# Performance work log

Measured on AMD Instinct MI355X. Metric: run time of the kernel, lower is better.

The kernel has to match this reference:

```python
import jax, jax.numpy as jnp
import numpy as np
import math

# dims: batch, tgt_len, img_feat, wordvec, heads, vocab, layers, ffn
N, T, D, W, H, V, L, FF = 8, 512, 1024, 512, 4, 32000, 2, 2048
NULL = 0  # padding_idx -> zero embedding row


def _pos_encoding(max_len, dim):
    pos = jnp.arange(max_len, dtype=jnp.float32)[:, None]
    j = jnp.arange(dim)[None, :]
    je = (j - (j % 2)).astype(jnp.float32)
    ang = pos * jnp.power(10000.0, -je / dim)
    return jnp.where(j % 2 == 0, jnp.sin(ang), jnp.cos(ang))  # (max_len, dim)


def setup_inputs() -> dict:
    key = jax.random.key(0)
    ks = iter(jax.random.split(key, 80))

    def nrm(shape):
        return jax.random.normal(next(ks), shape, jnp.float32) * 0.02

    inp = {}
    inp["features"] = jax.random.normal(next(ks), (N, D), jnp.float32)
    inp["captions"] = jax.random.randint(next(ks), (N, T), 0, V)
    emb = nrm((V, W)).at[NULL].set(0.0)  # padding_idx row zeroed
    inp["emb"] = emb
    inp["pe"] = _pos_encoding(T, W)
    inp["vis_w"] = nrm((D, W)); inp["vis_b"] = jnp.zeros((W,), jnp.float32)
    for p in ["sa", "ca"]:
        for q in ["q", "k", "v", "o"]:
            inp[f"{p}_w{q}"] = nrm((L, W, W))
            inp[f"{p}_b{q}"] = jnp.zeros((L, W), jnp.float32)
    inp["ff1_w"] = nrm((L, W, FF)); inp["ff1_b"] = jnp.zeros((L, FF), jnp.float32)
    inp["ff2_w"] = nrm((L, FF, W)); inp["ff2_b"] = jnp.zeros((L, W), jnp.float32)
    for i in (1, 2, 3):
        inp[f"ln{i}_w"] = jnp.ones((L, W), jnp.float32)
        inp[f"ln{i}_b"] = jnp.zeros((L, W), jnp.float32)
    inp["out_w"] = nrm((W, V)); inp["out_b"] = jnp.zeros((V,), jnp.float32)
    return inp


def _layer_norm(x, w, b):
    m = x.mean(-1, keepdims=True)
    v = ((x - m) ** 2).mean(-1, keepdims=True)
    return (x - m) / jnp.sqrt(v + 1e-5) * w + b


def _mha(qx, kx, vx, wq, bq, wk, bk, wv, bv, wo, bo, mask):
    n, s, e = qx.shape
    t = kx.shape[1]
    d = e // H
    q = (qx @ wq + bq).reshape(n, s, H, d)
    k = (kx @ wk + bk).reshape(n, t, H, d)
    v = (vx @ wv + bv).reshape(n, t, H, d)
    a = jnp.einsum("nshd,nthd->nhst", q, k) / math.sqrt(d)  # (N,H,S,T)
    if mask is not None:
        a = jnp.where(mask, a, -jnp.inf)
    e_ = jax.nn.softmax(a, axis=-1)
    y = jnp.einsum("nhst,nthd->nshd", e_, v).reshape(n, s, e)
    return y @ wo + bo


def reference(features, captions, emb, pe, vis_w, vis_b,
              sa_wq, sa_bq, sa_wk, sa_bk, sa_wv, sa_bv, sa_wo, sa_bo,
              ca_wq, ca_bq, ca_wk, ca_bk, ca_wv, ca_bv, ca_wo, ca_bo,
              ff1_w, ff1_b, ff2_w, ff2_b,
              ln1_w, ln1_b, ln2_w, ln2_b, ln3_w, ln3_b, out_w, out_b):
    memory = (features @ vis_w + vis_b)[:, None, :]  # (N,1,W)
    t_len = captions.shape[1]
    x = emb[captions] + pe[None, :t_len, :]  # (N,T,W)
    mask = jnp.tril(jnp.ones((t_len, t_len), bool))  # causal tgt_mask
    for l in range(L):
        t2 = _mha(x, x, x, sa_wq[l], sa_bq[l], sa_wk[l], sa_bk[l],
                  sa_wv[l], sa_bv[l], sa_wo[l], sa_bo[l], mask)
        x = _layer_norm(x + t2, ln1_w[l], ln1_b[l])
        t2 = _mha(x, memory, memory, ca_wq[l], ca_bq[l], ca_wk[l], ca_bk[l],
                  ca_wv[l], ca_bv[l], ca_wo[l], ca_bo[l], None)
        x = _layer_norm(x + t2, ln2_w[l], ln2_b[l])
        t2 = jax.nn.relu(x @ ff1_w[l] + ff1_b[l]) @ ff2_w[l] + ff2_b[l]
        x = _layer_norm(x + t2, ln3_w[l], ln3_b[l])
    return x @ out_w + out_b  # (N,T,V)
```

## Files before the change

### kernel.cpp

```cpp
#include <hip/hip_runtime.h>
#include <math.h>

#define WDIM   512
#define TLEN   512
#define NBATCH 8
#define NHEADS 4
#define DHEAD  128
#define VOCAB  32000
#define NLAY   2
#define FFDIM  2048
#define DFEAT  1024
#define NT     (NBATCH * TLEN)
#define QKVW   (3 * WDIM)

typedef unsigned short u16;
typedef __attribute__((ext_vector_type(8))) short bf16x8;
typedef __attribute__((ext_vector_type(4))) float f32x4;

__device__ inline u16 f2bf(float f) {
    union { float f; unsigned u; } v; v.f = f;
    unsigned r = v.u + 0x7fffu + ((v.u >> 16) & 1u);
    return (u16)(r >> 16);
}
__device__ inline u16 to_bf(float f) { return f2bf(f); }
__device__ inline u16 to_bf(u16 v)  { return v; }

__global__ __launch_bounds__(256)
void cvt_kernel(const float* __restrict__ s, u16* __restrict__ d, int n)
{
    int i = blockIdx.x * 256 + threadIdx.x;
    if (i < n) d[i] = f2bf(s[i]);
}

__global__ __launch_bounds__(256)
void concat_bias_kernel(const float* __restrict__ bq, const float* __restrict__ bk,
                        const float* __restrict__ bv, float* __restrict__ dst)
{
    int i = blockIdx.x * 256 + threadIdx.x;
    if (i >= NLAY * QKVW) return;
    int l = i / QKVW, j = i - l * QKVW;
    float v = (j < WDIM) ? bq[l * WDIM + j]
            : (j < 2 * WDIM) ? bk[l * WDIM + j - WDIM]
            : bv[l * WDIM + j - 2 * WDIM];
    dst[i] = v;
}

template<typename T>
__global__ __launch_bounds__(256)
void transpose_cvt_kernel(const T* __restrict__ src, int lds_, long ssn, long ssh,
                          u16* __restrict__ dst, int ldd, long dsn, long dsh,
                          int HH)
{
    int z = blockIdx.z;
    int zn = z / HH, zh = z - zn * HH;
    src += (long)zn * ssn + (long)zh * ssh;
    dst += (long)zn * dsn + (long)zh * dsh;
    __shared__ T tile[32][33];
    int n0 = blockIdx.x * 32, k0 = blockIdx.y * 32;
    int tx = threadIdx.x & 31, ty = threadIdx.x >> 5;
    #pragma unroll
    for (int i = 0; i < 32; i += 8)
        tile[ty + i][tx] = src[(long)(k0 + ty + i) * lds_ + n0 + tx];
    __syncthreads();
    #pragma unroll
    for (int i = 0; i < 32; i += 8)
        dst[(long)(n0 + ty + i) * ldd + k0 + tx] = to_bf(tile[tx][ty + i]);
}

__global__ __launch_bounds__(128)
void embed_kernel(const int* __restrict__ captions, const float* __restrict__ emb,
                  const float* __restrict__ pe, float* __restrict__ x, u16* __restrict__ xb)
{
    int r = blockIdx.x;
    int t = r % TLEN;
    int cap = captions[r];
    const float4* e4 = (const float4*)(emb + (long)cap * WDIM);
    const float4* p4 = (const float4*)(pe + (long)t * WDIM);
    float4 a = e4[threadIdx.x], b = p4[threadIdx.x];
    float4 o = make_float4(a.x + b.x, a.y + b.y, a.z + b.z, a.w + b.w);
    ((float4*)(x + (long)r * WDIM))[threadIdx.x] = o;
    ushort4 ob = make_ushort4(f2bf(o.x), f2bf(o.y), f2bf(o.z), f2bf(o.w));
    ((ushort4*)(xb + (long)r * WDIM))[threadIdx.x] = ob;
}

#define GBM 128
#define GBN 128
#define GBK 32

template<int RELU, int NTST, int CAUSAL>
__global__ __launch_bounds__(256)
void mfma_gemm_kernel(const u16* __restrict__ A, int lda, long sAn, long sAh,
                      const u16* __restrict__ B, int ldb, long sBn, long sBh,
                      float* __restrict__ C, u16* __restrict__ Cb, int ldc, long sCn, long sCh,
                      const float* __restrict__ bias, long sbias,
                      int M, int N, int K, int HH, float alpha)
{
    int z = blockIdx.z;
    int zn = z / HH, zh = z - zn * HH;
    A += (long)zn * sAn + (long)zh * sAh;
    B += (long)zn * sBn + (long)zh * sBh;
    long coff = (long)zn * sCn + (long)zh * sCh;
    if (bias) bias += (long)zn * sbias;

    int nwg  = gridDim.x * gridDim.y;
    int orig = blockIdx.y * gridDim.x + blockIdx.x;
    int q = nwg >> 3, r = nwg & 7, xcd = orig & 7, rest = orig >> 3;
    int nw = (xcd < r ? xcd * (q + 1) : r * (q + 1) + (xcd - r) * q) + rest;
    int bx = nw / gridDim.y, by = nw - bx * gridDim.y;
    int bm = by * GBM, bn = bx * GBN;

    if (CAUSAL && bn >= bm + GBM) return;

    __shared__ u16 As[2][GBM * GBK];
    __shared__ u16 Bs[2][GBN * GBK];

    int tid = threadIdx.x;
    int w = tid >> 6, lane = tid & 63;
    int wr = w >> 1, wc = w & 1;
    int lrow = lane & 15, kgrp = lane >> 4;

    int c0row = tid >> 2, c0ko = (tid & 3) << 3;
    long ldsOff = (size_t)(w * 64) * 8;

    auto STAGE = [&](int buf, int ks) {
        int k0 = ks * GBK;
        #pragma unroll
        for (int i = 0; i < 2; i++) {
            int row = c0row + i * 64;
            int gr = bm + row; if (gr >= M) gr = M - 1;
            const u16* srcA = A + (long)gr * lda + k0 + c0ko;
            u16* dstA = &As[buf][ldsOff + (size_t)i * 256 * 8];
            __builtin_amdgcn_global_load_lds((const __attribute__((address_space(1))) void*)srcA,
                                             (__attribute__((address_space(3))) void*)dstA, 16, 0, 0);
            const u16* srcB = B + (long)(bn + row) * ldb + k0 + c0ko;
            u16* dstB = &Bs[buf][ldsOff + (size_t)i * 256 * 8];
            __builtin_amdgcn_global_load_lds((const __attribute__((address_space(1))) void*)srcB,
                                             (__attribute__((address_space(3))) void*)dstB, 16, 0, 0);
        }
    };

    f32x4 acc[4][4] = {};
    int nsteps = K / GBK;

    STAGE(0, 0);

    for (int ks = 0; ks < nsteps; ks++) {
        int cur = ks & 1;
        if (ks + 1 < nsteps) {
            STAGE(cur ^ 1, ks + 1);
            asm volatile("s_waitcnt vmcnt(4)" ::: "memory");
        } else {
            asm volatile("s_waitcnt vmcnt(0)" ::: "memory");
        }
        __builtin_amdgcn_sched_barrier(0);
        __builtin_amdgcn_s_barrier();
        __builtin_amdgcn_sched_barrier(0);
        bf16x8 av[4], bv[4];
        #pragma unroll
        for (int m = 0; m < 4; m++)
            av[m] = *(const bf16x8*)&As[cur][(wr * 64 + m * 16 + lrow) * GBK + kgrp * 8];
        #pragma unroll
        for (int n = 0; n < 4; n++)
            bv[n] = *(const bf16x8*)&Bs[cur][(wc * 64 + n * 16 + lrow) * GBK + kgrp * 8];
        #pragma unroll
        for (int m = 0; m < 4; m++)
            #pragma unroll
            for (int n = 0; n < 4; n++)
                acc[m][n] = __builtin_amdgcn_mfma_f32_16x16x32_bf16(av[m], bv[n], acc[m][n], 0, 0, 0);
        __builtin_amdgcn_sched_barrier(0);
        __builtin_amdgcn_s_barrier();
        __builtin_amdgcn_sched_barrier(0);
    }

    if (NTST) {
        __syncthreads();
        float* ls = (float*)&As[0][0];
        C += coff;
        #pragma unroll
        for (int pass = 0; pass < 4; pass++) {
            if (wr == (pass >> 1)) {
                #pragma unroll
                for (int m2 = 0; m2 < 2; m2++) {
                    int m = (pass & 1) * 2 + m2;
                    #pragma unroll
                    for (int n = 0; n < 4; n++) {
                        int gc = wc * 64 + n * 16 + lrow;
                        float bvv = bias ? bias[bn + gc] : 0.f;
                        #pragma unroll
                        for (int r2 = 0; r2 < 4; r2++) {
                            float v2 = acc[m][n][r2] * alpha + bvv;
                            if (RELU) v2 = fmaxf(v2, 0.f);
                            ls[(m2 * 16 + kgrp * 4 + r2) * 128 + gc] = v2;
                        }
                    }
                }
            }
            __syncthreads();
            #pragma unroll
            for (int i = 0; i < 4; i++) {
                int j = tid + i * 256;
                int row = j >> 5, cg = j & 31;
                int gr = bm + pass * 32 + row;
                if (gr < M) {
                    f32x4 v4 = *(const f32x4*)&ls[row * 128 + cg * 4];
                    __builtin_nontemporal_store(v4, (f32x4*)&C[(long)gr * ldc + bn + cg * 4]);
                }
            }
            __syncthreads();
        }
        return;
    }

    if (C)  C  += coff;
    if (Cb) Cb += coff;
    #pragma unroll
    for (int m = 0; m < 4; m++) {
        int rb = bm + wr * 64 + m * 16 + kgrp * 4;
        #pragma unroll
        for (int n = 0; n < 4; n++) {
            int gc = bn + wc * 64 + n * 16 + lrow;
            float bvv = bias ? bias[gc] : 0.f;
            #pragma unroll
            for (int r2 = 0; r2 < 4; r2++) {
                int gr = rb + r2;
                if (gr < M) {
                    float v2 = acc[m][n][r2] * alpha + bvv;
                    if (RELU) v2 = fmaxf(v2, 0.f);
                    if (C)  C[(long)gr * ldc + gc]  = v2;
                    if (Cb) Cb[(long)gr * ldc + gc] = f2bf(v2);
                }
            }
        }
    }
}

__global__ __launch_bounds__(128)
void mfma_gemm_half_kernel(const u16* __restrict__ A, int lda, long sAn, long sAh,
                           const u16* __restrict__ B, int ldb, long sBn, long sBh,
                           float* __restrict__ C, u16* __restrict__ Cb, int ldc, long sCn, long sCh,
                           const float* __restrict__ bias,
                           int M, int N, int K, int HH, float alpha)
{
    int z = blockIdx.z;
    int zn = z / HH, zh = z - zn * HH;
    A += (long)zn * sAn + (long)zh * sAh;
    B += (long)zn * sBn + (long)zh * sBh;
    long coff = (long)zn * sCn + (long)zh * sCh;

    int nwg  = gridDim.x * gridDim.y;
    int orig = blockIdx.y * gridDim.x + blockIdx.x;
    int q = nwg >> 3, r = nwg & 7, xcd = orig & 7, rest = orig >> 3;
    int nw = (xcd < r ? xcd * (q + 1) : r * (q + 1) + (xcd - r) * q) + rest;
    int bx = nw / gridDim.y, by = nw - bx * gridDim.y;
    int bm = by * 128, bn = bx * 64;

    __shared__ u16 As[2][128 * GBK];
    __shared__ u16 Bs[2][64 * GBK];

    int tid = threadIdx.x;
    int w = tid >> 6, lane = tid & 63;
    int lrow = lane & 15, kgrp = lane >> 4;

    auto STAGE = [&](int buf, int ks) {
        int k0 = ks * GBK;
        #pragma unroll
        for (int i = 0; i < 4; i++) {
            int c = tid + i * 128;
            int row = c >> 2, ko2 = (c & 3) << 3;
            int gr = bm + row; if (gr >= M) gr = M - 1;
            const u16* srcA = A + (long)gr * lda + k0 + ko2;
            u16* dstA = &As[buf][(size_t)(i * 128 + w * 64) * 8];
            __builtin_amdgcn_global_load_lds((const __attribute__((address_space(1))) void*)srcA,
                                             (__attribute__((address_space(3))) void*)dstA, 16, 0, 0);
        }
        #pragma unroll
        for (int i = 0; i < 2; i++) {
            int c = tid + i * 128;
            int row = c >> 2, ko2 = (c & 3) << 3;
            const u16* srcB = B + (long)(bn + row) * ldb + k0 + ko2;
            u16* dstB = &Bs[buf][(size_t)(i * 128 + w * 64) * 8];
            __builtin_amdgcn_global_load_lds((const __attribute__((address_space(1))) void*)srcB,
                                             (__attribute__((address_space(3))) void*)dstB, 16, 0, 0);
        }
    };

    f32x4 acc[4][4] = {};
    int nsteps = K / GBK;

    STAGE(0, 0);

    for (int ks = 0; ks < nsteps; ks++) {
        int cur = ks & 1;
        if (ks + 1 < nsteps) {
            STAGE(cur ^ 1, ks + 1);
            asm volatile("s_waitcnt vmcnt(6)" ::: "memory");
        } else {
            asm volatile("s_waitcnt vmcnt(0)" ::: "memory");
        }
        __builtin_amdgcn_sched_barrier(0);
        __builtin_amdgcn_s_barrier();
        __builtin_amdgcn_sched_barrier(0);
        bf16x8 av[4], bv[4];
        #pragma unroll
        for (int m = 0; m < 4; m++)
            av[m] = *(const bf16x8*)&As[cur][(w * 64 + m * 16 + lrow) * GBK + kgrp * 8];
        #pragma unroll
        for (int n = 0; n < 4; n++)
            bv[n] = *(const bf16x8*)&Bs[cur][(n * 16 + lrow) * GBK + kgrp * 8];
        #pragma unroll
        for (int m = 0; m < 4; m++)
            #pragma unroll
            for (int n = 0; n < 4; n++)
                acc[m][n] = __builtin_amdgcn_mfma_f32_16x16x32_bf16(av[m], bv[n], acc[m][n], 0, 0, 0);
        __builtin_amdgcn_sched_barrier(0);
        __builtin_amdgcn_s_barrier();
        __builtin_amdgcn_sched_barrier(0);
    }

    if (C)  C  += coff;
    if (Cb) Cb += coff;
    #pragma unroll
    for (int m = 0; m < 4; m++) {
        int rb = bm + w * 64 + m * 16 + kgrp * 4;
        #pragma unroll
        for (int n = 0; n < 4; n++) {
            int gc = bn + n * 16 + lrow;
            float bvv = bias ? bias[gc] : 0.f;
            #pragma unroll
            for (int r2 = 0; r2 < 4; r2++) {
                int gr = rb + r2;
                if (gr < M) {
                    float v2 = acc[m][n][r2] * alpha + bvv;
                    if (C)  C[(long)gr * ldc + gc]  = v2;
                    if (Cb) Cb[(long)gr * ldc + gc] = f2bf(v2);
                }
            }
        }
    }
}

__global__ __launch_bounds__(256)
void softmax_causal_kernel(const float* __restrict__ scores, u16* __restrict__ pb)
{
    long row = blockIdx.x;
    int s = (int)(row % TLEN);
    const float* p = scores + row * TLEN;
    u16* o = pb + row * TLEN;
    int tid = threadIdx.x;
    float v0 = p[tid], v1 = p[tid + 256];
    bool m0 = (tid <= s), m1 = (tid + 256 <= s);
    __shared__ float red[256];
    float mx = fmaxf(m0 ? v0 : -INFINITY, m1 ? v1 : -INFINITY);
    red[tid] = mx; __syncthreads();
    for (int off = 128; off > 0; off >>= 1) {
        if (tid < off) red[tid] = fmaxf(red[tid], red[tid + off]);
        __syncthreads();
    }
    mx = red[0]; __syncthreads();
    float e0 = m0 ? expf(v0 - mx) : 0.f;
    float e1 = m1 ? expf(v1 - mx) : 0.f;
    red[tid] = e0 + e1; __syncthreads();
    for (int off = 128; off > 0; off >>= 1) {
        if (tid < off) red[tid] += red[tid + off];
        __syncthreads();
    }
    float inv = 1.f / red[0];
    o[tid]       = f2bf(e0 * inv);
    o[tid + 256] = f2bf(e1 * inv);
}

__device__ inline void ln_pass(float& v0, float& v1, const float* __restrict__ w,
                               const float* __restrict__ b, float* red, int tid)
{
    red[tid] = v0 + v1; __syncthreads();
    for (int off = 128; off > 0; off >>= 1) {
        if (tid < off) red[tid] += red[tid + off];
        __syncthreads();
    }
    float mean = red[0] * (1.f / WDIM); __syncthreads();
    float d0 = v0 - mean, d1 = v1 - mean;
    red[tid] = d0 * d0 + d1 * d1; __syncthreads();
    for (int off = 128; off > 0; off >>= 1) {
        if (tid < off) red[tid] += red[tid + off];
        __syncthreads();
    }
    float rstd = 1.f / sqrtf(red[0] * (1.f / WDIM) + 1e-5f);
    __syncthreads();
    v0 = d0 * rstd * w[tid] + b[tid];
    v1 = d1 * rstd * w[tid + 256] + b[tid + 256];
}

__global__ __launch_bounds__(256)
void add_ln_kernel(float* __restrict__ x, u16* __restrict__ xb,
                   const float* __restrict__ t2,
                   const float* __restrict__ w, const float* __restrict__ b)
{
    long r = blockIdx.x;
    float* xr = x + r * WDIM;
    u16* xbr = xb + r * WDIM;
    const float* tr = t2 + r * WDIM;
    int tid = threadIdx.x;
    float v0 = xr[tid] + tr[tid];
    float v1 = xr[tid + 256] + tr[tid + 256];
    __shared__ float red[256];
    ln_pass(v0, v1, w, b, red, tid);
    xr[tid] = v0;        xr[tid + 256] = v1;
    xbr[tid] = f2bf(v0); xbr[tid + 256] = f2bf(v1);
}

__global__ __launch_bounds__(256)
void add_ln2_kernel(float* __restrict__ x, u16* __restrict__ xb,
                    const float* __restrict__ t2, const float* __restrict__ cav,
                    const float* __restrict__ w1, const float* __restrict__ b1,
                    const float* __restrict__ w2, const float* __restrict__ b2)
{
    long r = blockIdx.x;
    float* xr = x + r * WDIM;
    u16* xbr = xb + r * WDIM;
    const float* tr = t2 + r * WDIM;
    const float* cr = cav + (r / TLEN) * WDIM;
    int tid = threadIdx.x;
    float v0 = xr[tid] + tr[tid];
    float v1 = xr[tid + 256] + tr[tid + 256];
    __shared__ float red[256];
    ln_pass(v0, v1, w1, b1, red, tid);
    __syncthreads();
    v0 += cr[tid]; v1 += cr[tid + 256];
    ln_pass(v0, v1, w2, b2, red, tid);
    xr[tid] = v0;        xr[tid + 256] = v1;
    xbr[tid] = f2bf(v0); xbr[tid + 256] = f2bf(v1);
}

extern "C" void kernel_launch(void* const* d_in, const int* in_sizes, int n_in,
                              void* d_out, int out_size, void* d_ws, size_t ws_size,
                              hipStream_t stream)
{
    const float* features = (const float*)d_in[0];
    const int*   captions = (const int*)  d_in[1];
    const float* emb      = (const float*)d_in[2];
    const float* pe       = (const float*)d_in[3];
    const float* vis_w    = (const float*)d_in[4];
    const float* vis_b    = (const float*)d_in[5];
    const float* sa_wq    = (const float*)d_in[6];
    const float* sa_bq    = (const float*)d_in[7];
    const float* sa_wk    = (const float*)d_in[8];
    const float* sa_bk    = (const float*)d_in[9];
    const float* sa_wv    = (const float*)d_in[10];
    const float* sa_bv    = (const float*)d_in[11];
    const float* sa_wo    = (const float*)d_in[12];
    const float* sa_bo    = (const float*)d_in[13];
    const float* ca_wv    = (const float*)d_in[18];
    const float* ca_bv    = (const float*)d_in[19];
    const float* ca_wo    = (const float*)d_in[20];
    const float* ca_bo    = (const float*)d_in[21];
    const float* ff1_w    = (const float*)d_in[22];
    const float* ff1_b    = (const float*)d_in[23];
    const float* ff2_w    = (const float*)d_in[24];
    const float* ff2_b    = (const float*)d_in[25];
    const float* ln1_w    = (const float*)d_in[26];
    const float* ln1_b    = (const float*)d_in[27];
    const float* ln2_w    = (const float*)d_in[28];
    const float* ln2_b    = (const float*)d_in[29];
    const float* ln3_w    = (const float*)d_in[30];
    const float* ln3_b    = (const float*)d_in[31];
    const float* out_w    = (const float*)d_in[32];
    const float* out_b    = (const float*)d_in[33];

    char* p = (char*)d_ws;
    auto alloc = [&](size_t bytes) { char* r = p; p += (bytes + 255) & ~(size_t)255; return r; };
    float* x    = (float*)alloc((size_t)NT * WDIM * 4);
    float* t2   = (float*)alloc((size_t)NT * WDIM * 4);
    float* memb = (float*)alloc((size_t)NBATCH * WDIM * 4);
    float* cav  = (float*)alloc((size_t)NLAY * NBATCH * WDIM * 4);
    char*  reg1 = alloc((size_t)NBATCH * NHEADS * TLEN * TLEN * 4);
    float* scores = (float*)reg1;
    u16*   yb     = (u16*)reg1;
    u16*   hb     = (u16*)reg1;
    u16* xb    = (u16*)alloc((size_t)NT * WDIM * 2);
    u16* qkvb  = (u16*)alloc((size_t)NT * QKVW * 2);
    u16* vtb   = (u16*)alloc((size_t)NT * WDIM * 2);
    u16* pb    = (u16*)alloc((size_t)NBATCH * NHEADS * TLEN * TLEN * 2);
    u16* featb = (u16*)alloc((size_t)NBATCH * DFEAT * 2);
    u16* membf = (u16*)alloc((size_t)NBATCH * WDIM * 2);
    u16* cvb   = (u16*)alloc((size_t)NLAY * NBATCH * WDIM * 2);
    float* qkv_bias = (float*)alloc((size_t)NLAY * QKVW * 4);
    u16* vis_wT = (u16*)alloc((size_t)WDIM * DFEAT * 2);
    u16* qkvT   = (u16*)alloc((size_t)NLAY * QKVW * WDIM * 2);
    u16* sa_woT = (u16*)alloc((size_t)NLAY * WDIM * WDIM * 2);
    u16* ca_wvT = (u16*)alloc((size_t)NLAY * WDIM * WDIM * 2);
    u16* ca_woT = (u16*)alloc((size_t)NLAY * WDIM * WDIM * 2);
    u16* ff1T   = (u16*)alloc((size_t)NLAY * WDIM * FFDIM * 2);
    u16* ff2T   = (u16*)alloc((size_t)NLAY * FFDIM * WDIM * 2);
    u16* out_wT = (u16*)alloc((size_t)WDIM * VOCAB * 2);

    auto gemm = [&](const u16* A, int lda, long sAn, long sAh,
                    const u16* B, int ldb, long sBn, long sBh,
                    float* C, u16* Cb, int ldc, long sCn, long sCh,
                    const float* bias, long sbias, int M, int N, int K, int HH, int batch,
                    float alpha, int mode)
    {
        dim3 g(N / GBN, (M + GBM - 1) / GBM, batch), blk(256);
        if (mode == 2)
            mfma_gemm_kernel<0, 1, 0><<<g, blk, 0, stream>>>(A, lda, sAn, sAh, B, ldb, sBn, sBh,
                                                             C, Cb, ldc, sCn, sCh, bias, sbias, M, N, K, HH, alpha);
        else if (mode == 1)
            mfma_gemm_kernel<1, 0, 0><<<g, blk, 0, stream>>>(A, lda, sAn, sAh, B, ldb, sBn, sBh,
                                                             C, Cb, ldc, sCn, sCh, bias, sbias, M, N, K, HH, alpha);
        else if (mode == 3)
            mfma_gemm_kernel<0, 0, 1><<<g, blk, 0, stream>>>(A, lda, sAn, sAh, B, ldb, sBn, sBh,
                                                             C, Cb, ldc, sCn, sCh, bias, sbias, M, N, K, HH, alpha);
        else
            mfma_gemm_kernel<0, 0, 0><<<g, blk, 0, stream>>>(A, lda, sAn, sAh, B, ldb, sBn, sBh,
                                                             C, Cb, ldc, sCn, sCh, bias, sbias, M, N, K, HH, alpha);
    };
    auto gemmh = [&](const u16* A, int lda, long sAn, long sAh,
                     const u16* B, int ldb, long sBn, long sBh,
                     float* C, u16* Cb, int ldc, long sCn, long sCh,
                     const float* bias, int M, int N, int K, int HH, int batch,
                     float alpha)
    {
        dim3 g(N / 64, (M + 127) / 128, batch), blk(128);
        mfma_gemm_half_kernel<<<g, blk, 0, stream>>>(A, lda, sAn, sAh, B, ldb, sBn, sBh,
                                                     C, Cb, ldc, sCn, sCh, bias, M, N, K, HH, alpha);
    };
    auto transposeF = [&](const float* src, int lds_, long ssn, long ssh,
                          u16* dst, int ldd, long dsn, long dsh,
                          int K, int N, int batch, int HH)
    {
        dim3 g(N / 32, K / 32, batch), blk(256);
        transpose_cvt_kernel<float><<<g, blk, 0, stream>>>(src, lds_, ssn, ssh, dst, ldd, dsn, dsh, HH);
    };
    auto transposeB = [&](const u16* src, int lds_, long ssn, long ssh,
                          u16* dst, int ldd, long dsn, long dsh,
                          int K, int N, int batch, int HH)
    {
        dim3 g(N / 32, K / 32, batch), blk(256);
        transpose_cvt_kernel<u16><<<g, blk, 0, stream>>>(src, lds_, ssn, ssh, dst, ldd, dsn, dsh, HH);
    };

    cvt_kernel<<<(NBATCH * DFEAT + 255) / 256, 256, 0, stream>>>(features, featb, NBATCH * DFEAT);
    concat_bias_kernel<<<(NLAY * QKVW + 255) / 256, 256, 0, stream>>>(sa_bq, sa_bk, sa_bv, qkv_bias);
    transposeF(vis_w, WDIM, 0, 0, vis_wT, DFEAT, 0, 0, DFEAT, WDIM, 1, 1);
    transposeF(sa_wq, WDIM, (long)WDIM * WDIM, 0, qkvT,                WDIM, (long)QKVW * WDIM, 0, WDIM, WDIM, NLAY, 1);
    transposeF(sa_wk, WDIM, (long)WDIM * WDIM, 0, qkvT + (long)WDIM * WDIM,     WDIM, (long)QKVW * WDIM, 0, WDIM, WDIM, NLAY, 1);
    transposeF(sa_wv, WDIM, (long)WDIM * WDIM, 0, qkvT + (long)2 * WDIM * WDIM, WDIM, (long)QKVW * WDIM, 0, WDIM, WDIM, NLAY, 1);
    transposeF(sa_wo, WDIM, (long)WDIM * WDIM, 0, sa_woT, WDIM, (long)WDIM * WDIM, 0, WDIM, WDIM, NLAY, 1);
    transposeF(ca_wv, WDIM, (long)WDIM * WDIM, 0, ca_wvT, WDIM, (long)WDIM * WDIM, 0, WDIM, WDIM, NLAY, 1);
    transposeF(ca_wo, WDIM, (long)WDIM * WDIM, 0, ca_woT, WDIM, (long)WDIM * WDIM, 0, WDIM, WDIM, NLAY, 1);
    transposeF(ff1_w, FFDIM, (long)WDIM * FFDIM, 0, ff1T, WDIM, (long)FFDIM * WDIM, 0, WDIM, FFDIM, NLAY, 1);
    transposeF(ff2_w, WDIM, (long)FFDIM * WDIM, 0, ff2T, FFDIM, (long)WDIM * FFDIM, 0, FFDIM, WDIM, NLAY, 1);
    transposeF(out_w, VOCAB, 0, 0, out_wT, WDIM, 0, 0, WDIM, VOCAB, 1, 1);

    gemm(featb, DFEAT, 0, 0, vis_wT, DFEAT, 0, 0, memb, membf, WDIM, 0, 0,
         vis_b, 0, NBATCH, WDIM, DFEAT, 1, 1, 1.f, 0);
    embed_kernel<<<NT, 128, 0, stream>>>(captions, emb, pe, x, xb);

    gemm(membf, WDIM, 0, 0, ca_wvT, WDIM, (long)WDIM * WDIM, 0,
         nullptr, cvb, WDIM, (long)NBATCH * WDIM, 0,
         ca_bv, WDIM, NBATCH, WDIM, WDIM, 1, NLAY, 1.f, 0);
    gemm(cvb, WDIM, (long)NBATCH * WDIM, 0, ca_woT, WDIM, (long)WDIM * WDIM, 0,
         cav, nullptr, WDIM, (long)NBATCH * WDIM, 0,
         ca_bo, WDIM, NBATCH, WDIM, WDIM, 1, NLAY, 1.f, 0);

    const float iscale = 1.f / sqrtf((float)DHEAD);
    const long TQ = (long)TLEN * QKVW;
    const long TW = (long)TLEN * WDIM;
    const long TT = (long)TLEN * TLEN;
    for (int l = 0; l < NLAY; l++) {
        long wo  = (long)l * WDIM * WDIM;
        long bo_ = (long)l * WDIM;
        gemm(xb, WDIM, 0, 0, qkvT + (long)l * QKVW * WDIM, WDIM, 0, 0,
             nullptr, qkvb, QKVW, 0, 0, qkv_bias + (long)l * QKVW, 0,
             NT, QKVW, WDIM, 1, 1, 1.f, 0);
        transposeB(qkvb + 2 * WDIM, QKVW, TQ, DHEAD,
                   vtb, TLEN, (long)NHEADS * DHEAD * TLEN, (long)DHEAD * TLEN,
                   TLEN, DHEAD, NBATCH * NHEADS, NHEADS);
        gemm(qkvb, QKVW, TQ, DHEAD, qkvb + WDIM, QKVW, TQ, DHEAD,
             scores, nullptr, TLEN, (long)NHEADS * TT, TT,
             nullptr, 0, TLEN, TLEN, DHEAD, NHEADS, NBATCH * NHEADS, iscale, 3);
        softmax_causal_kernel<<<NBATCH * NHEADS * TLEN, 256, 0, stream>>>(scores, pb);
        gemmh(pb, TLEN, (long)NHEADS * TT, TT,
              vtb, TLEN, (long)NHEADS * DHEAD * TLEN, (long)DHEAD * TLEN,
              nullptr, yb, WDIM, TW, DHEAD,
              nullptr, TLEN, DHEAD, TLEN, NHEADS, NBATCH * NHEADS, 1.f);
        gemmh(yb, WDIM, 0, 0, sa_woT + wo, WDIM, 0, 0, t2, nullptr, WDIM, 0, 0,
              sa_bo + bo_, NT, WDIM, WDIM, 1, 1, 1.f);
        add_ln2_kernel<<<NT, 256, 0, stream>>>(x, xb, t2, cav + (long)l * NBATCH * WDIM,
                                               ln1_w + bo_, ln1_b + bo_, ln2_w + bo_, ln2_b + bo_);
        gemm(xb, WDIM, 0, 0, ff1T + (long)l * FFDIM * WDIM, WDIM, 0, 0,
             nullptr, hb, FFDIM, 0, 0, ff1_b + (long)l * FFDIM, 0,
             NT, FFDIM, WDIM, 1, 1, 1.f, 1);
        gemmh(hb, FFDIM, 0, 0, ff2T + (long)l * WDIM * FFDIM, FFDIM, 0, 0,
              t2, nullptr, WDIM, 0, 0, ff2_b + bo_, NT, WDIM, FFDIM, 1, 1, 1.f);
        add_ln_kernel<<<NT, 256, 0, stream>>>(x, xb, t2, ln3_w + bo_, ln3_b + bo_);
    }
    gemm(xb, WDIM, 0, 0, out_wT, WDIM, 0, 0, (float*)d_out, nullptr, VOCAB, 0, 0,
         out_b, 0, NT, VOCAB, WDIM, 1, 1, 1.f, 2);
}
```

Measured before the change: 732.1 us.

## Add 256x256-tile GEMM with LDS-staged nontemporal stores for vocab projection

Adds a dedicated 512-thread kernel for the final vocabulary projection (4096x32000x512). It uses 256x256 output tiles with double-buffered direct global-to-LDS loads, and stages results through LDS so that fp32 output rows are written with coalesced 16-byte nontemporal stores. The goal is more operand reuse per block and better write efficiency for the large fp32 logits output, which is likely bandwidth-bound. The larger tile costs more registers and fewer blocks (125x16 grid), and mode 2 of the generic path is removed.

New measurement: 720.4 us, median of 2. Within noise of the previous version (-1.6%).

```diff
diff --git a/kernel.cpp b/kernel.cpp
--- a/kernel.cpp
+++ b/kernel.cpp
@@ -234,6 +234,116 @@
     }
 }
 
+__global__ __launch_bounds__(512)
+void mfma_gemm256_nt_kernel(const u16* __restrict__ A, int lda,
+                            const u16* __restrict__ B, int ldb,
+                            float* __restrict__ C, int ldc,
+                            const float* __restrict__ bias,
+                            int M, int N, int K, float alpha)
+{
+    int nwg  = gridDim.x * gridDim.y;
+    int orig = blockIdx.y * gridDim.x + blockIdx.x;
+    int q = nwg >> 3, r = nwg & 7, xcd = orig & 7, rest = orig >> 3;
+    int nw = (xcd < r ? xcd * (q + 1) : r * (q + 1) + (xcd - r) * q) + rest;
+    int bx = nw / gridDim.y, by = nw - bx * gridDim.y;
+    int bm = by * 256, bn = bx * 256;
+
+    __shared__ u16 smem[4 * 256 * 32];
+
+    int tid = threadIdx.x;
+    int w = tid >> 6, lane = tid & 63;
+    int wr = w >> 2, wc = w & 3;
+    int lrow = lane & 15, kgrp = lane >> 4;
+
+    int c0row = tid >> 2, c0ko = (tid & 3) << 3;
+
+    auto STAGE = [&](int buf, int ks) {
+        int k0 = ks * GBK;
+        #pragma unroll
+        for (int i = 0; i < 2; i++) {
+            int row = c0row + i * 128;
+            int gr = bm + row; if (gr >= M) gr = M - 1;
+            const u16* srcA = A + (long)gr * lda + k0 + c0ko;
+            u16* dstA = &smem[(size_t)buf * 8192 + (size_t)(i * 512 + w * 64) * 8];
+            __builtin_amdgcn_global_load_lds((const __attribute__((address_space(1))) void*)srcA,
+                                             (__attribute__((address_space(3))) void*)dstA, 16, 0, 0);
+            const u16* srcB = B + (long)(bn + row) * ldb + k0 + c0ko;
+            u16* dstB = &smem[16384 + (size_t)buf * 8192 + (size_t)(i * 512 + w * 64) * 8];
+            __builtin_amdgcn_global_load_lds((const __attribute__((address_space(1))) void*)srcB,
+                                             (__attribute__((address_space(3))) void*)dstB, 16, 0, 0);
+        }
+    };
+
+    f32x4 acc[8][4] = {};
+    int nsteps = K / GBK;
+
+    STAGE(0, 0);
+
+    for (int ks = 0; ks < nsteps; ks++) {
+        int cur = ks & 1;
+        if (ks + 1 < nsteps) {
+            STAGE(cur ^ 1, ks + 1);
+            asm volatile("s_waitcnt vmcnt(4)" ::: "memory");
+        } else {
+            asm volatile("s_waitcnt vmcnt(0)" ::: "memory");
+        }
+        __builtin_amdgcn_sched_barrier(0);
+        __builtin_amdgcn_s_barrier();
+        __builtin_amdgcn_sched_barrier(0);
+        const u16* Asb = &smem[(size_t)cur * 8192];
+        const u16* Bsb = &smem[16384 + (size_t)cur * 8192];
+        bf16x8 av[8], bv[4];
+        #pragma unroll
+        for (int m = 0; m < 8; m++)
+            av[m] = *(const bf16x8*)&Asb[(wr * 128 + m * 16 + lrow) * GBK + kgrp * 8];
+        #pragma unroll
+        for (int n = 0; n < 4; n++)
+            bv[n] = *(const bf16x8*)&Bsb[(wc * 64 + n * 16 + lrow) * GBK + kgrp * 8];
+        #pragma unroll
+        for (int m = 0; m < 8; m++)
+            #pragma unroll
+            for (int n = 0; n < 4; n++)
+                acc[m][n] = __builtin_amdgcn_mfma_f32_16x16x32_bf16(av[m], bv[n], acc[m][n], 0, 0, 0);
+        __builtin_amdgcn_sched_barrier(0);
+        __builtin_amdgcn_s_barrier();
+        __builtin_amdgcn_sched_barrier(0);
+    }
+
+    __syncthreads();
+    float* ls = (float*)smem;
+    #pragma unroll
+    for (int pass = 0; pass < 4; pass++) {
+        if (wr == (pass >> 1)) {
+            #pragma unroll
+            for (int m2 = 0; m2 < 4; m2++) {
+                int m = (pass & 1) * 4 + m2;
+                #pragma unroll
+                for (int n = 0; n < 4; n++) {
+                    int gc = wc * 64 + n * 16 + lrow;
+                    float bvv = bias ? bias[bn + gc] : 0.f;
+                    #pragma unroll
+                    for (int r2 = 0; r2 < 4; r2++) {
+                        float v2 = acc[m][n][r2] * alpha + bvv;
+                        ls[(m2 * 16 + kgrp * 4 + r2) * 256 + gc] = v2;
+                    }
+                }
+            }
+        }
+        __syncthreads();
+        #pragma unroll
+        for (int i = 0; i < 8; i++) {
+            int j = tid + i * 512;
+            int row = j >> 6, cg = j & 63;
+            int gr = bm + pass * 64 + row;
+            if (gr < M) {
+                f32x4 v4 = *(const f32x4*)&ls[row * 256 + cg * 4];
+                __builtin_nontemporal_store(v4, (f32x4*)&C[(long)gr * ldc + bn + cg * 4]);
+            }
+        }
+        __syncthreads();
+    }
+}
+
 __global__ __launch_bounds__(128)
 void mfma_gemm_half_kernel(const u16* __restrict__ A, int lda, long sAn, long sAh,
                            const u16* __restrict__ B, int ldb, long sBn, long sBh,
@@ -500,10 +610,7 @@
                     float alpha, int mode)
     {
         dim3 g(N / GBN, (M + GBM - 1) / GBM, batch), blk(256);
-        if (mode == 2)
-            mfma_gemm_kernel<0, 1, 0><<<g, blk, 0, stream>>>(A, lda, sAn, sAh, B, ldb, sBn, sBh,
-                                                             C, Cb, ldc, sCn, sCh, bias, sbias, M, N, K, HH, alpha);
-        else if (mode == 1)
+        if (mode == 1)
             mfma_gemm_kernel<1, 0, 0><<<g, blk, 0, stream>>>(A, lda, sAn, sAh, B, ldb, sBn, sBh,
                                                              C, Cb, ldc, sCn, sCh, bias, sbias, M, N, K, HH, alpha);
         else if (mode == 3)
@@ -594,6 +701,10 @@
               t2, nullptr, WDIM, 0, 0, ff2_b + bo_, NT, WDIM, FFDIM, 1, 1, 1.f);
         add_ln_kernel<<<NT, 256, 0, stream>>>(x, xb, t2, ln3_w + bo_, ln3_b + bo_);
     }
-    gemm(xb, WDIM, 0, 0, out_wT, WDIM, 0, 0, (float*)d_out, nullptr, VOCAB, 0, 0,
-         out_b, 0, NT, VOCAB, WDIM, 1, 1, 1.f, 2);
-}
+    {
+        dim3 g(VOCAB / 256, NT / 256, 1), blk(512);
+        mfma_gemm256_nt_kernel<<<g, blk, 0, stream>>>(xb, WDIM, out_wT, WDIM,
+                                                      (float*)d_out, VOCAB, out_b,
+                                                      NT, VOCAB, WDIM, 1.f);
+    }
+}
```
